# Optimization experiments

Hardware: AMD Instinct MI355X
Metric: run time of the kernel (lower is better)

Reference implementation:

```python
import jax, jax.numpy as jnp
import numpy as np

GROUP = 32  # hadamard group size == MX block size


def _hadamard(n):
    H = np.array([[1.0]], dtype=np.float64)
    while H.shape[0] < n:
        H = np.block([[H, H], [H, -H]])
    return (H * n ** -0.5).astype(np.float32)


def _fp4_e2m1_rne(v):
    # round-to-nearest-even onto {0, 0.5, 1, 1.5, 2, 3, 4, 6} (signed)
    s = jnp.sign(v)
    a = jnp.minimum(jnp.abs(v), 6.0)
    e = jnp.clip(jnp.floor(jnp.log2(jnp.maximum(a, 2.0 ** -10))), 0.0, 2.0)
    step = jnp.exp2(e - 1.0)  # 0.5 / 1 / 2 depending on binade
    return s * jnp.round(a / step) * step  # jnp.round is half-to-even


def _mxfp4_quant_dequant(t):
    # blockwise MXFP4 with power-of-two (E8M0) shared scale per 32 elems
    shp = t.shape
    tb = t.reshape(-1, GROUP)
    amax = jnp.max(jnp.abs(tb), axis=-1, keepdims=True)
    # shared exponent: floor(log2(amax)) - emax_fp4 (=2, since max e2m1 = 6.0)
    scale = jnp.exp2(jnp.floor(jnp.log2(jnp.maximum(amax, 1e-30))) - 2.0)
    scale = jnp.where(amax > 0, scale, 1.0)
    return (_fp4_e2m1_rne(tb / scale) * scale).reshape(shp)


def _rotate(t, hadamard):
    g = hadamard.shape[0]
    return (t.reshape(-1, g) @ hadamard).reshape(t.shape)


def setup_inputs() -> dict:
    key = jax.random.key(0)
    k1, k2, k3 = jax.random.split(key, 3)
    tokens, in_f, out_f = 8192, 4096, 16384
    x = jax.random.normal(k1, (tokens, in_f), dtype=jnp.float32)
    weight = jax.random.normal(k2, (out_f, in_f), dtype=jnp.float32) * (in_f ** -0.5)
    bias = jax.random.normal(k3, (out_f,), dtype=jnp.float32) * 0.01
    hadamard = jnp.asarray(_hadamard(GROUP))
    return {"x": x, "weight": weight, "bias": bias, "hadamard": hadamard}


def reference(x, weight, bias, hadamard) -> jnp.ndarray:
    # pre_forward: dqweight = dequant(mxfp4_quant(hadamard_rotate(weight)))
    w_dq = _mxfp4_quant_dequant(_rotate(weight, hadamard))
    # forward: x -> hadamard rotate -> mxfp4 pseudoquant -> matmul -> +bias
    x_dq = _mxfp4_quant_dequant(_rotate(x, hadamard))
    return x_dq @ w_dq.T + bias
```

## Files before the change

kernel.cpp:

```cpp
#include <hip/hip_runtime.h>
#include <stdint.h>

typedef float v4f  __attribute__((ext_vector_type(4)));
typedef float v16f __attribute__((ext_vector_type(16)));
typedef int   v4i  __attribute__((ext_vector_type(4)));
typedef int   v8i  __attribute__((ext_vector_type(8)));

__device__ __forceinline__ void gload_lds16(const void* g, void* l) {
  __builtin_amdgcn_global_load_lds(
      (const __attribute__((address_space(1))) void*)g,
      (__attribute__((address_space(3))) void*)l, 16, 0, 0);
}
__device__ __forceinline__ void gload_lds4(const void* g, void* l) {
  __builtin_amdgcn_global_load_lds(
      (const __attribute__((address_space(1))) void*)g,
      (__attribute__((address_space(3))) void*)l, 4, 0, 0);
}

__global__ __launch_bounds__(256) void quant_fp4_kernel(
    const float* __restrict__ in, uint32_t* __restrict__ packed,
    uint8_t* __restrict__ scales, int R, int rshift) {
  int g = blockIdx.x * 256 + threadIdx.x;
  int kb = g >> rshift, row = g & (R - 1);

  float v[32];
  const v4f* p = (const v4f*)(in + (size_t)row * 4096 + kb * 32);
#pragma unroll
  for (int c = 0; c < 8; ++c) {
    v4f t = p[c];
    v[c * 4 + 0] = t[0]; v[c * 4 + 1] = t[1];
    v[c * 4 + 2] = t[2]; v[c * 4 + 3] = t[3];
  }
#pragma unroll
  for (int s = 0; s < 5; ++s) {
    const int h = 1 << s;
#pragma unroll
    for (int k = 0; k < 16; ++k) {
      const int i = ((k >> s) << (s + 1)) | (k & (h - 1));
      float a = v[i], b = v[i + h];
      v[i] = a + b; v[i + h] = a - b;
    }
  }
  const float RS = 0.17677669529663687f;
  float amax = 0.0f;
#pragma unroll
  for (int i = 0; i < 32; ++i) {
    v[i] *= RS;
    amax = fmaxf(amax, fabsf(v[i]));
  }
  int E;
  float rscale;
  if (amax > 0.0f) {
    float am = fmaxf(amax, 1e-30f);
    E = (int)((__float_as_uint(am) >> 23) & 255u) - 127;
    rscale = __uint_as_float((uint32_t)(2 - E + 127) << 23);
  } else { E = 2; rscale = 1.0f; }

  uint32_t dw[4] = {0u, 0u, 0u, 0u};
#pragma unroll
  for (int i = 0; i < 32; ++i) {
    float x = v[i];
    float a = fminf(fabsf(x) * rscale, 6.0f);
    float rstep = a >= 4.0f ? 0.5f : (a >= 2.0f ? 1.0f : 2.0f);
    float step  = a >= 4.0f ? 2.0f : (a >= 2.0f ? 1.0f : 0.5f);
    float q = rintf(a * rstep) * step;
    uint32_t uq = __float_as_uint(q);
    int Eq = (int)(uq >> 23) - 127;
    uint32_t code = (q == 0.0f) ? 0u
                  : (Eq < 0 ? 1u
                            : (((uint32_t)(Eq + 1) << 1) | ((uq >> 22) & 1u)));
    code |= (__float_as_uint(x) >> 31) << 3;
    dw[i >> 3] |= code << (4 * (i & 7));
  }
  uint4 o; o.x = dw[0]; o.y = dw[1]; o.z = dw[2]; o.w = dw[3];
  *(uint4*)(packed + (size_t)g * 4) = o;

  int kt = kb >> 3, hik = kb & 1, ks = (kb >> 1) & 3;
  scales[(size_t)((kt * 2 + hik) * R + row) * 4 + ks] = (uint8_t)(E - 2 + 127);
}

#define MFMA4(a, b, c, sa, sb) \
  __builtin_amdgcn_mfma_scale_f32_32x32x64_f8f6f4((a), (b), (c), 4, 4, 0, (sa), 0, (sb))
#define BARRIER { asm volatile("" ::: "memory"); __builtin_amdgcn_s_barrier(); asm volatile("" ::: "memory"); }
#define LGKM0  asm volatile("s_waitcnt lgkmcnt(0)" ::: "memory")
#define VMW(n) asm volatile("s_waitcnt vmcnt(" #n ")" ::: "memory")

__device__ __forceinline__ v8i frag4(const uint8_t* p) {
  v4i lo = *(const v4i*)p;
  v8i r;
  r[0] = lo[0]; r[1] = lo[1]; r[2] = lo[2]; r[3] = lo[3];
  r[4] = 0; r[5] = 0; r[6] = 0; r[7] = 0;
  return r;
}

__global__ __launch_bounds__(512, 2) void gemm_fp4_8ph(
    const uint8_t* __restrict__ Apk, const uint8_t* __restrict__ Bpk,
    const uint32_t* __restrict__ Asc, const uint32_t* __restrict__ Bsc,
    const float* __restrict__ bias, float* __restrict__ C) {
  const int N = 16384;
  __shared__ uint8_t lds[139264];

  const int tid = threadIdx.x, lane = tid & 63, wv = tid >> 6;
  const int wm = wv >> 2, wn = wv & 3;
  const int hi = lane >> 5, r32 = lane & 31;

  const int bid = blockIdx.x;
  const int xcd = bid & 7, idx = bid >> 3, st = idx >> 5;
  const int mT = ((st & 3) * 8 + (idx & 7)) * 256;
  const int nT = (xcd * 8 + (st >> 2) * 4 + ((idx >> 3) & 3)) * 256;

  const int sOp = wv >> 2;
  const int sR2 = (wv >> 1) & 1;
  const int s0  = 2 * (wv & 1);
  const uint8_t* opBase = sOp ? Bpk : Apk;
  const size_t RB = sOp ? (size_t)16384 * 16 : (size_t)8192 * 16;
  const int T0 = sOp ? nT : mT;
  const size_t gOff0 = (size_t)(T0 + (s0 + 0) * 64 + lane) * 16;
  const size_t gOff1 = (size_t)(T0 + (s0 + 1) * 64 + lane) * 16;
  const int dOff0 = sOp * 32768 + sR2 * 4096 + (s0 + 0) * 1024 + lane * 16;
  const int dOff1 = sOp * 32768 + sR2 * 4096 + (s0 + 1) * 1024 + lane * 16;

  auto STG_OPS = [&](int kt, int a, int bb) {
    const uint8_t* g0 = opBase + (size_t)(kt * 8 + a + sR2) * RB;
    uint8_t* l = &lds[bb * 65536 + a * 4096];
    gload_lds16(g0 + gOff0, l + dOff0);
    gload_lds16(g0 + gOff1, l + dOff1);
  };

  const uint32_t* scBase = sOp ? Bsc : Asc;
  const int Rrows = sOp ? 16384 : 8192;
  auto STG_SC = [&](int kt, int bb) {
    const uint32_t* g = scBase + (size_t)(kt * 2 + sR2) * Rrows + T0;
    uint8_t* l = &lds[131072 + bb * 4096 + sOp * 2048 + sR2 * 1024];
    gload_lds4(g + (s0 + 0) * 64 + lane, l + (s0 + 0) * 256 + lane * 4);
    gload_lds4(g + (s0 + 1) * 64 + lane, l + (s0 + 1) * 256 + lane * 4);
  };

  const int aRd = hi * 4096 + (wm * 128 + r32) * 16;
  const int bRd = 32768 + hi * 4096 + (wn * 64 + r32) * 16;
  const int aSc = 131072 + hi * 1024 + (wm * 128 + r32) * 4;
  const int bSc = 131072 + 2048 + hi * 1024 + (wn * 64 + r32) * 4;

  v16f acc[4][2] = {};
  uint32_t saD[4], sbD[2];

#define FRAGS(bb, j) \
    v8i fA[4], fB[2]; \
    _Pragma("unroll") for (int mf = 0; mf < 4; ++mf) \
      fA[mf] = frag4(&lds[(bb) * 65536 + (j) * 8192 + aRd + mf * 512]); \
    _Pragma("unroll") for (int nf = 0; nf < 2; ++nf) \
      fB[nf] = frag4(&lds[(bb) * 65536 + (j) * 8192 + bRd + nf * 512]);

#define SCRD(bb) \
    _Pragma("unroll") for (int mf = 0; mf < 4; ++mf) \
      saD[mf] = *(const uint32_t*)&lds[(bb) * 4096 + aSc + mf * 128]; \
    _Pragma("unroll") for (int nf = 0; nf < 2; ++nf) \
      sbD[nf] = *(const uint32_t*)&lds[(bb) * 4096 + bSc + nf * 128];

#define MM8(j) \
    __builtin_amdgcn_s_setprio(1); \
    _Pragma("unroll") for (int mf = 0; mf < 4; ++mf) \
    _Pragma("unroll") for (int nf = 0; nf < 2; ++nf) \
      acc[mf][nf] = MFMA4(fA[mf], fB[nf], acc[mf][nf], \
                          (int)((saD[mf] >> (8 * (j))) & 255u), \
                          (int)((sbD[nf] >> (8 * (j))) & 255u)); \
    __builtin_amdgcn_s_setprio(0);

#define PH(bb, j, ISSUE, WAITBAR) { \
    FRAGS(bb, j); \
    if ((j) == 0) { SCRD(bb); } \
    ISSUE; \
    BARRIER; LGKM0; \
    MM8(j); \
    WAITBAR; }

  STG_OPS(0, 0, 0); STG_OPS(0, 2, 0); STG_OPS(0, 4, 0); STG_OPS(0, 6, 0);
  STG_SC(0, 0);
  STG_OPS(1, 0, 1); STG_OPS(1, 2, 1); STG_OPS(1, 4, 1);
  STG_SC(1, 1);
  VMW(8);
  BARRIER;

#pragma unroll 1
  for (int i = 0; i < 7; ++i) {
    const int t0 = 2 * i;
    PH(0, 0, { STG_OPS(t0 + 1, 6, 1); },                       BARRIER);
    PH(0, 1, { STG_OPS(t0 + 2, 0, 0); STG_SC(t0 + 2, 0); },    BARRIER);
    PH(0, 2, { STG_OPS(t0 + 2, 2, 0); },                       BARRIER);
    PH(0, 3, { STG_OPS(t0 + 2, 4, 0); },                       { VMW(8); BARRIER; });
    PH(1, 0, { STG_OPS(t0 + 2, 6, 0); },                       BARRIER);
    PH(1, 1, { STG_OPS(t0 + 3, 0, 1); STG_SC(t0 + 3, 1); },    BARRIER);
    PH(1, 2, { STG_OPS(t0 + 3, 2, 1); },                       BARRIER);
    PH(1, 3, { STG_OPS(t0 + 3, 4, 1); },                       { VMW(8); BARRIER; });
  }
  PH(0, 0, { STG_OPS(15, 6, 1); }, BARRIER);
  PH(0, 1, {;},                    BARRIER);
  PH(0, 2, {;},                    BARRIER);
  PH(0, 3, {;},                    { VMW(0); BARRIER; });
  PH(1, 0, {;},                    BARRIER);
  PH(1, 1, {;},                    BARRIER);
  PH(1, 2, {;},                    BARRIER);
  PH(1, 3, {;},                    {;});

#pragma unroll
  for (int nf = 0; nf < 2; ++nf) {
    const int col = nT + wn * 64 + nf * 32 + r32;
    const float bv = bias[col];
#pragma unroll
    for (int mf = 0; mf < 4; ++mf) {
      const int rbase = mT + wm * 128 + mf * 32 + 4 * hi;
#pragma unroll
      for (int q = 0; q < 16; ++q) {
        const int rowl = (q & 3) + 8 * (q >> 2);
        C[(size_t)(rbase + rowl) * N + col] = acc[mf][nf][q] + bv;
      }
    }
  }
}

extern "C" void kernel_launch(void* const* d_in, const int* in_sizes, int n_in,
                              void* d_out, int out_size, void* d_ws, size_t ws_size,
                              hipStream_t stream) {
  const float* x    = (const float*)d_in[0];
  const float* w    = (const float*)d_in[1];
  const float* bias = (const float*)d_in[2];
  float* out = (float*)d_out;

  uint8_t* x_pk = (uint8_t*)d_ws;
  uint8_t* w_pk = x_pk + (size_t)16 * 1024 * 1024;
  uint8_t* x_sc = w_pk + (size_t)32 * 1024 * 1024;
  uint8_t* w_sc = x_sc + (size_t)1  * 1024 * 1024;

  quant_fp4_kernel<<<4096, 256, 0, stream>>>(x, (uint32_t*)x_pk, x_sc, 8192, 13);
  quant_fp4_kernel<<<8192, 256, 0, stream>>>(w, (uint32_t*)w_pk, w_sc, 16384, 14);

  gemm_fp4_8ph<<<2048, dim3(512), 0, stream>>>(
      x_pk, w_pk, (const uint32_t*)x_sc, (const uint32_t*)w_sc, bias, out);
}
```

Before: 484.4 us.

## Double-buffer LDS fragment registers to prefetch next k-phase during MFMA

Restructures the GEMM main loop so each tile's four k-phases use two alternating register fragment sets. The next phase's LDS reads are issued before the current phase's MFMAs, and partial lgkmcnt waits replace full drains. Sched barriers pin the instruction order, and the fragments are padded with undefined lanes instead of zero-filled. This aims to hide LDS read latency behind matrix work at the cost of more VGPRs, which may pressure the 2-wave occupancy target.

After: 486.6 us. About the same (+0.5%).

```diff
diff --git a/kernel.cpp b/kernel.cpp
--- a/kernel.cpp
+++ b/kernel.cpp
@@ -81,17 +81,11 @@
 
 #define MFMA4(a, b, c, sa, sb) \
   __builtin_amdgcn_mfma_scale_f32_32x32x64_f8f6f4((a), (b), (c), 4, 4, 0, (sa), 0, (sb))
+#define PAD8(x) __builtin_shufflevector((x), (x), 0, 1, 2, 3, -1, -1, -1, -1)
 #define BARRIER { asm volatile("" ::: "memory"); __builtin_amdgcn_s_barrier(); asm volatile("" ::: "memory"); }
-#define LGKM0  asm volatile("s_waitcnt lgkmcnt(0)" ::: "memory")
-#define VMW(n) asm volatile("s_waitcnt vmcnt(" #n ")" ::: "memory")
-
-__device__ __forceinline__ v8i frag4(const uint8_t* p) {
-  v4i lo = *(const v4i*)p;
-  v8i r;
-  r[0] = lo[0]; r[1] = lo[1]; r[2] = lo[2]; r[3] = lo[3];
-  r[4] = 0; r[5] = 0; r[6] = 0; r[7] = 0;
-  return r;
-}
+#define SB0 __builtin_amdgcn_sched_barrier(0)
+#define LGKM(n) { asm volatile("s_waitcnt lgkmcnt(" #n ")" ::: "memory"); SB0; }
+#define VMW(n)  asm volatile("s_waitcnt vmcnt(" #n ")" ::: "memory")
 
 __global__ __launch_bounds__(512, 2) void gemm_fp4_8ph(
     const uint8_t* __restrict__ Apk, const uint8_t* __restrict__ Bpk,
@@ -136,43 +130,53 @@
     gload_lds4(g + (s0 + 1) * 64 + lane, l + (s0 + 1) * 256 + lane * 4);
   };
 
-  const int aRd = hi * 4096 + (wm * 128 + r32) * 16;
-  const int bRd = 32768 + hi * 4096 + (wn * 64 + r32) * 16;
-  const int aSc = 131072 + hi * 1024 + (wm * 128 + r32) * 4;
-  const int bSc = 131072 + 2048 + hi * 1024 + (wn * 64 + r32) * 4;
+  const int aRd0 = hi * 4096 + (wm * 128 + r32) * 16;
+  const int aRd1 = aRd0 + 65536;
+  const int bRd0 = 32768 + hi * 4096 + (wn * 64 + r32) * 16;
+  const int bRd1 = bRd0 + 65536;
+  const int aSc0 = 131072 + hi * 1024 + (wm * 128 + r32) * 4;
+  const int aSc1 = aSc0 + 4096;
+  const int bSc0 = 131072 + 2048 + hi * 1024 + (wn * 64 + r32) * 4;
+  const int bSc1 = bSc0 + 4096;
 
   v16f acc[4][2] = {};
+  v4i fA0[4], fB0[2], fA1[4], fB1[2];
   uint32_t saD[4], sbD[2];
 
-#define FRAGS(bb, j) \
-    v8i fA[4], fB[2]; \
+#define LDF(FA, FB, ARD, BRD, j) { \
     _Pragma("unroll") for (int mf = 0; mf < 4; ++mf) \
-      fA[mf] = frag4(&lds[(bb) * 65536 + (j) * 8192 + aRd + mf * 512]); \
+      FA[mf] = *(const v4i*)&lds[(ARD) + (j) * 8192 + mf * 512]; \
     _Pragma("unroll") for (int nf = 0; nf < 2; ++nf) \
-      fB[nf] = frag4(&lds[(bb) * 65536 + (j) * 8192 + bRd + nf * 512]);
-
-#define SCRD(bb) \
+      FB[nf] = *(const v4i*)&lds[(BRD) + (j) * 8192 + nf * 512]; }
+
+#define SCRD(ASC, BSC) { \
     _Pragma("unroll") for (int mf = 0; mf < 4; ++mf) \
-      saD[mf] = *(const uint32_t*)&lds[(bb) * 4096 + aSc + mf * 128]; \
+      saD[mf] = *(const uint32_t*)&lds[(ASC) + mf * 128]; \
     _Pragma("unroll") for (int nf = 0; nf < 2; ++nf) \
-      sbD[nf] = *(const uint32_t*)&lds[(bb) * 4096 + bSc + nf * 128];
-
-#define MM8(j) \
+      sbD[nf] = *(const uint32_t*)&lds[(BSC) + nf * 128]; }
+
+#define MM8(FA, FB, j) { \
     __builtin_amdgcn_s_setprio(1); \
     _Pragma("unroll") for (int mf = 0; mf < 4; ++mf) \
     _Pragma("unroll") for (int nf = 0; nf < 2; ++nf) \
-      acc[mf][nf] = MFMA4(fA[mf], fB[nf], acc[mf][nf], \
+      acc[mf][nf] = MFMA4(PAD8(FA[mf]), PAD8(FB[nf]), acc[mf][nf], \
                           (int)((saD[mf] >> (8 * (j))) & 255u), \
                           (int)((sbD[nf] >> (8 * (j))) & 255u)); \
-    __builtin_amdgcn_s_setprio(0);
-
-#define PH(bb, j, ISSUE, WAITBAR) { \
-    FRAGS(bb, j); \
-    if ((j) == 0) { SCRD(bb); } \
-    ISSUE; \
-    BARRIER; LGKM0; \
-    MM8(j); \
-    WAITBAR; }
+    __builtin_amdgcn_s_setprio(0); }
+
+#define TILE(bb, t, ARD, BRD, ASC, BSC, ob) { \
+    SCRD(ASC, BSC); LDF(fA0, fB0, ARD, BRD, 0); SB0; LDF(fA1, fB1, ARD, BRD, 1); \
+    STG_OPS((t) + 1, 6, ob); \
+    BARRIER; LGKM(6); MM8(fA0, fB0, 0); BARRIER; \
+    LDF(fA0, fB0, ARD, BRD, 2); \
+    STG_OPS((t) + 2, 0, bb); STG_SC((t) + 2, bb); \
+    BARRIER; LGKM(6); MM8(fA1, fB1, 1); BARRIER; \
+    LDF(fA1, fB1, ARD, BRD, 3); \
+    STG_OPS((t) + 2, 2, bb); \
+    BARRIER; LGKM(6); MM8(fA0, fB0, 2); BARRIER; \
+    STG_OPS((t) + 2, 4, bb); \
+    BARRIER; LGKM(0); MM8(fA1, fB1, 3); \
+    VMW(8); BARRIER; }
 
   STG_OPS(0, 0, 0); STG_OPS(0, 2, 0); STG_OPS(0, 4, 0); STG_OPS(0, 6, 0);
   STG_SC(0, 0);
@@ -184,23 +188,27 @@
 #pragma unroll 1
   for (int i = 0; i < 7; ++i) {
     const int t0 = 2 * i;
-    PH(0, 0, { STG_OPS(t0 + 1, 6, 1); },                       BARRIER);
-    PH(0, 1, { STG_OPS(t0 + 2, 0, 0); STG_SC(t0 + 2, 0); },    BARRIER);
-    PH(0, 2, { STG_OPS(t0 + 2, 2, 0); },                       BARRIER);
-    PH(0, 3, { STG_OPS(t0 + 2, 4, 0); },                       { VMW(8); BARRIER; });
-    PH(1, 0, { STG_OPS(t0 + 2, 6, 0); },                       BARRIER);
-    PH(1, 1, { STG_OPS(t0 + 3, 0, 1); STG_SC(t0 + 3, 1); },    BARRIER);
-    PH(1, 2, { STG_OPS(t0 + 3, 2, 1); },                       BARRIER);
-    PH(1, 3, { STG_OPS(t0 + 3, 4, 1); },                       { VMW(8); BARRIER; });
-  }
-  PH(0, 0, { STG_OPS(15, 6, 1); }, BARRIER);
-  PH(0, 1, {;},                    BARRIER);
-  PH(0, 2, {;},                    BARRIER);
-  PH(0, 3, {;},                    { VMW(0); BARRIER; });
-  PH(1, 0, {;},                    BARRIER);
-  PH(1, 1, {;},                    BARRIER);
-  PH(1, 2, {;},                    BARRIER);
-  PH(1, 3, {;},                    {;});
+    TILE(0, t0,     aRd0, bRd0, aSc0, bSc0, 1);
+    TILE(1, t0 + 1, aRd1, bRd1, aSc1, bSc1, 0);
+  }
+
+  SCRD(aSc0, bSc0); LDF(fA0, fB0, aRd0, bRd0, 0); SB0; LDF(fA1, fB1, aRd0, bRd0, 1);
+  STG_OPS(15, 6, 1);
+  BARRIER; LGKM(6); MM8(fA0, fB0, 0); BARRIER;
+  LDF(fA0, fB0, aRd0, bRd0, 2);
+  BARRIER; LGKM(6); MM8(fA1, fB1, 1); BARRIER;
+  LDF(fA1, fB1, aRd0, bRd0, 3);
+  BARRIER; LGKM(6); MM8(fA0, fB0, 2); BARRIER;
+  BARRIER; LGKM(0); MM8(fA1, fB1, 3);
+  VMW(0); BARRIER;
+
+  SCRD(aSc1, bSc1); LDF(fA0, fB0, aRd1, bRd1, 0); SB0; LDF(fA1, fB1, aRd1, bRd1, 1);
+  BARRIER; LGKM(6); MM8(fA0, fB0, 0); BARRIER;
+  LDF(fA0, fB0, aRd1, bRd1, 2);
+  BARRIER; LGKM(6); MM8(fA1, fB1, 1); BARRIER;
+  LDF(fA1, fB1, aRd1, bRd1, 3);
+  BARRIER; LGKM(6); MM8(fA0, fB0, 2); BARRIER;
+  BARRIER; LGKM(0); MM8(fA1, fB1, 3);
 
 #pragma unroll
   for (int nf = 0; nf < 2; ++nf) {
```
